# Kernel tuning notes

Hardware: AMD Instinct MI355X
Metric: run time of the kernel (lower is better)

The kernel has to match this reference:

```python
import jax, jax.numpy as jnp
import numpy as np

EPS = 1e-7
NUM_ROUTINGS = 3


def squash(s):
    # s: [..., V]; maps norm into [0, 1)
    norm = jnp.linalg.norm(s, axis=-1, keepdims=True)
    coef = norm ** 2 / (norm ** 2 + 1.0)
    return coef * s / (norm + EPS)


def setup_inputs() -> dict:
    key = jax.random.key(0)
    k1, k2 = jax.random.split(key)
    B, N, Q = 32, 32768, 8          # batch, num_primary, dim_primary
    D, V = 10, 16                   # num_digit, dim_digit
    primary_caps = jax.random.normal(k1, (B, N, Q), dtype=jnp.float32)
    # glorot-ish scale for W [num_digit, num_primary, dim_digit, dim_primary]
    W = jax.random.normal(k2, (D, N, V, Q), dtype=jnp.float32) * (1.0 / np.sqrt(Q))
    return {"primary_caps": primary_caps, "W": W}


def reference(primary_caps, W):
    # u_hat[b,d,n,v] = sum_q W[d,n,v,q] * u[b,n,q]  -> [B, D, N, V]
    u_hat = jnp.einsum("dnvq,bnq->bdnv", W, primary_caps)
    B, D, N, V = u_hat.shape
    b = jnp.zeros((B, D, N), dtype=u_hat.dtype)
    v = None
    for r in range(NUM_ROUTINGS):
        c = jax.nn.softmax(b, axis=1)                      # softmax over digit axis
        s = jnp.einsum("bdn,bdnv->bdv", c, u_hat)          # [B, D, V]
        v = squash(s)                                      # [B, D, V]
        if r < NUM_ROUTINGS - 1:
            b = b + jnp.einsum("bdnv,bdv->bdn", u_hat, v)  # agreement update
    return v  # [B, num_digit, dim_digit]
```

## Files before the change

kernel.cpp:

```cpp
#include <hip/hip_runtime.h>

namespace {
constexpr int kB = 32;
constexpr int kN = 32768;
constexpr int kQ = 8;
constexpr int kD = 10;
constexpr int kV = 16;
constexpr int kRows = kB * kD;
constexpr int kThreads = 512;
constexpr int kGrid = 1024;
constexpr int kNPB = kN / kGrid;
}

template <int CTRL>
__device__ __forceinline__ float dpp_mv(float x) {
  return __int_as_float(__builtin_amdgcn_update_dpp(
      0, __float_as_int(x), CTRL, 0xF, 0xF, true));
}

template <int PHASE>
__launch_bounds__(kThreads, 2)
__global__ void routing_pass(const float* __restrict__ u,
                             const float* __restrict__ W,
                             const float* __restrict__ vprev,
                             float* __restrict__ s_out) {
  const int t = threadIdx.x;
  const int ln = t & 63;
  const int dslot = ln >> 2;
  const int vq = ln & 3;
  const bool act = (dslot < kD);
  const int dd = act ? dslot : dslot - kD;
  const int b0 = (t >> 6) * 4;

  float vp[4][4];
  if constexpr (PHASE != 0) {
    #pragma unroll
    for (int bb = 0; bb < 4; ++bb)
      #pragma unroll
      for (int j = 0; j < 4; ++j)
        vp[bb][j] = vprev[((b0 + bb) * kD + dd) * kV + j * 4 + vq];
  }

  float acc[4][4];
  #pragma unroll
  for (int bb = 0; bb < 4; ++bb)
    #pragma unroll
    for (int j = 0; j < 4; ++j) acc[bb][j] = 0.0f;

  const int n_base = blockIdx.x * kNPB;
  const char* wbase = (const char*)W + ((size_t)dd * kN + n_base) * 512 + vq * 32;
  const int ub = b0 + ((ln & 31) >> 3);
  const float* ubase = u + ((size_t)ub * kN + n_base + (ln >> 5)) * kQ + (ln & 7);

  for (int g = 0; g < kNPB / 4; ++g) {
    const float r0 = ubase[(g * 4 + 0) * kQ];
    const float r1 = ubase[(g * 4 + 2) * kQ];
    #pragma unroll
    for (int nl = 0; nl < 4; ++nl) {
      const float upair = (nl < 2) ? r0 : r1;
      const int hb = (nl & 1) * 32;
      const char* wn = wbase + (size_t)(g * 4 + nl) * 512;

      float uh[4][4];
      #pragma unroll
      for (int bb = 0; bb < 4; ++bb)
        #pragma unroll
        for (int j = 0; j < 4; ++j) uh[bb][j] = 0.0f;

      #pragma unroll
      for (int qh = 0; qh < 2; ++qh) {
        float us[4][4];
        #pragma unroll
        for (int bb = 0; bb < 4; ++bb)
          #pragma unroll
          for (int ql = 0; ql < 4; ++ql)
            us[bb][ql] = __int_as_float(__builtin_amdgcn_readlane(
                __float_as_int(upair), hb + bb * 8 + qh * 4 + ql));
        #pragma unroll
        for (int j = 0; j < 4; ++j) {
          const float4 w4 = *(const float4*)(wn + j * 128 + qh * 16);
          #pragma unroll
          for (int bb = 0; bb < 4; ++bb) {
            uh[bb][j] = fmaf(w4.x, us[bb][0], uh[bb][j]);
            uh[bb][j] = fmaf(w4.y, us[bb][1], uh[bb][j]);
            uh[bb][j] = fmaf(w4.z, us[bb][2], uh[bb][j]);
            uh[bb][j] = fmaf(w4.w, us[bb][3], uh[bb][j]);
          }
        }
      }
      if constexpr (PHASE != 0) {
        float lg[4];
        #pragma unroll
        for (int bb = 0; bb < 4; ++bb) {
          float t0 = uh[bb][0] * vp[bb][0];
          t0 = fmaf(uh[bb][1], vp[bb][1], t0);
          t0 = fmaf(uh[bb][2], vp[bb][2], t0);
          t0 = fmaf(uh[bb][3], vp[bb][3], t0);
          t0 += dpp_mv<0xB1>(t0);
          t0 += dpp_mv<0x4E>(t0);
          lg[bb] = t0;
        }
        const float ta = (vq & 2) ? lg[2] : lg[0];
        const float tb = (vq & 2) ? lg[3] : lg[1];
        const float lsel = (vq & 1) ? tb : ta;
        const float esel = act ? __expf(lsel) : 0.0f;
        float den = esel;
        den += dpp_mv<0x124>(den);
        den += dpp_mv<0x128>(den);
        den += __shfl_xor(den, 16);
        den += __shfl_xor(den, 32);
        const float csel = esel * __builtin_amdgcn_rcpf(den);
        const float cb[4] = {dpp_mv<0x00>(csel), dpp_mv<0x55>(csel),
                             dpp_mv<0xAA>(csel), dpp_mv<0xFF>(csel)};
        #pragma unroll
        for (int bb = 0; bb < 4; ++bb)
          #pragma unroll
          for (int j = 0; j < 4; ++j)
            acc[bb][j] = fmaf(cb[bb], uh[bb][j], acc[bb][j]);
      } else {
        #pragma unroll
        for (int bb = 0; bb < 4; ++bb)
          #pragma unroll
          for (int j = 0; j < 4; ++j) acc[bb][j] += uh[bb][j];
      }
    }
  }

  if (act) {
    const float scale = (PHASE == 0) ? 0.1f : 1.0f;
    #pragma unroll
    for (int bb = 0; bb < 4; ++bb) {
      float* srow = s_out + ((b0 + bb) * kD + dslot) * kV + vq;
      #pragma unroll
      for (int j = 0; j < 4; ++j)
        atomicAdd(&srow[j * 4], acc[bb][j] * scale);
    }
  }
}

template <int MODE>
__global__ void squash_kernel(float* __restrict__ s,
                              float* __restrict__ vprev,
                              float* __restrict__ out) {
  const int t = threadIdx.x;
  if (t >= kRows) return;
  float* sr = s + t * kV;
  float sv[kV];
  float n2 = 0.0f;
  #pragma unroll
  for (int v = 0; v < kV; ++v) {
    sv[v] = sr[v];
    n2 = fmaf(sv[v], sv[v], n2);
  }
  if (MODE != 2) {
    #pragma unroll
    for (int v = 0; v < kV; ++v) sr[v] = 0.0f;
  }
  const float norm = sqrtf(n2);
  const float coef = n2 / ((n2 + 1.0f) * (norm + 1e-7f));
  float* dst = (MODE == 2) ? (out + t * kV) : (vprev + t * kV);
  #pragma unroll
  for (int v = 0; v < kV; ++v) {
    float val = coef * sv[v];
    if (MODE == 1) val += dst[v];
    dst[v] = val;
  }
}

extern "C" void kernel_launch(void* const* d_in, const int* in_sizes, int n_in,
                              void* d_out, int out_size, void* d_ws, size_t ws_size,
                              hipStream_t stream) {
  const float* u = reinterpret_cast<const float*>(d_in[0]);
  const float* W = reinterpret_cast<const float*>(d_in[1]);
  float* out = reinterpret_cast<float*>(d_out);

  float* s = reinterpret_cast<float*>(d_ws);
  float* vprev = s + kRows * kV;
  const size_t sbytes = (size_t)kRows * kV * sizeof(float);

  (void)hipMemsetAsync(s, 0, sbytes, stream);
  routing_pass<0><<<kGrid, kThreads, 0, stream>>>(u, W, nullptr, s);
  squash_kernel<0><<<1, kThreads, 0, stream>>>(s, vprev, out);

  routing_pass<1><<<kGrid, kThreads, 0, stream>>>(u, W, vprev, s);
  squash_kernel<1><<<1, kThreads, 0, stream>>>(s, vprev, out);

  routing_pass<1><<<kGrid, kThreads, 0, stream>>>(u, W, vprev, s);
  squash_kernel<2><<<1, kThreads, 0, stream>>>(s, vprev, out);
}
```

Before: 618.7 us.

## Split batch across two blocks per N-partition to halve per-thread register tiles

Each block now handles 16 of the 32 batch rows (2 per wave instead of 4), doubling the grid and halving accumulator and u_hat register arrays, with launch bounds raised to 4 blocks per CU. This aims to improve occupancy and latency hiding. The cost is that every W tile is read twice (once per batch half), doubling W traffic, plus more atomics to the output.

```diff
diff --git a/kernel.cpp b/kernel.cpp
--- a/kernel.cpp
+++ b/kernel.cpp
@@ -8,8 +8,10 @@
 constexpr int kV = 16;
 constexpr int kRows = kB * kD;
 constexpr int kThreads = 512;
-constexpr int kGrid = 1024;
-constexpr int kNPB = kN / kGrid;
+constexpr int kParts = 1024;
+constexpr int kGrid = kParts * 2;
+constexpr int kNPB = kN / kParts;
+constexpr int kG = kNPB / 4;
 }
 
 template <int CTRL>
@@ -19,7 +21,7 @@
 }
 
 template <int PHASE>
-__launch_bounds__(kThreads, 2)
+__launch_bounds__(kThreads, 4)
 __global__ void routing_pass(const float* __restrict__ u,
                              const float* __restrict__ W,
                              const float* __restrict__ vprev,
@@ -30,57 +32,55 @@
   const int vq = ln & 3;
   const bool act = (dslot < kD);
   const int dd = act ? dslot : dslot - kD;
-  const int b0 = (t >> 6) * 4;
+  const int bg = blockIdx.x & 1;
+  const int part = blockIdx.x >> 1;
+  const int b0 = bg * 16 + (t >> 6) * 2;
+  const int n_base = part * kNPB;
 
-  float vp[4][4];
+  float vp[2][4];
   if constexpr (PHASE != 0) {
     #pragma unroll
-    for (int bb = 0; bb < 4; ++bb)
+    for (int bb = 0; bb < 2; ++bb)
       #pragma unroll
       for (int j = 0; j < 4; ++j)
         vp[bb][j] = vprev[((b0 + bb) * kD + dd) * kV + j * 4 + vq];
   }
 
-  float acc[4][4];
+  float acc[2][4];
   #pragma unroll
-  for (int bb = 0; bb < 4; ++bb)
+  for (int bb = 0; bb < 2; ++bb)
     #pragma unroll
     for (int j = 0; j < 4; ++j) acc[bb][j] = 0.0f;
 
-  const int n_base = blockIdx.x * kNPB;
   const char* wbase = (const char*)W + ((size_t)dd * kN + n_base) * 512 + vq * 32;
-  const int ub = b0 + ((ln & 31) >> 3);
-  const float* ubase = u + ((size_t)ub * kN + n_base + (ln >> 5)) * kQ + (ln & 7);
+  const float* ubase = u + ((size_t)(b0 + (ln >> 5)) * kN + n_base + ((ln >> 3) & 3)) * kQ
+                       + (ln & 7);
 
-  for (int g = 0; g < kNPB / 4; ++g) {
-    const float r0 = ubase[(g * 4 + 0) * kQ];
-    const float r1 = ubase[(g * 4 + 2) * kQ];
+  for (int g = 0; g < kG; ++g) {
+    const float ureg = ubase[g * 4 * kQ];
     #pragma unroll
     for (int nl = 0; nl < 4; ++nl) {
-      const float upair = (nl < 2) ? r0 : r1;
-      const int hb = (nl & 1) * 32;
       const char* wn = wbase + (size_t)(g * 4 + nl) * 512;
-
-      float uh[4][4];
+      float uh[2][4];
       #pragma unroll
-      for (int bb = 0; bb < 4; ++bb)
+      for (int bb = 0; bb < 2; ++bb)
         #pragma unroll
         for (int j = 0; j < 4; ++j) uh[bb][j] = 0.0f;
 
       #pragma unroll
       for (int qh = 0; qh < 2; ++qh) {
-        float us[4][4];
+        float us[2][4];
         #pragma unroll
-        for (int bb = 0; bb < 4; ++bb)
+        for (int bb = 0; bb < 2; ++bb)
           #pragma unroll
           for (int ql = 0; ql < 4; ++ql)
             us[bb][ql] = __int_as_float(__builtin_amdgcn_readlane(
-                __float_as_int(upair), hb + bb * 8 + qh * 4 + ql));
+                __float_as_int(ureg), bb * 32 + nl * 8 + qh * 4 + ql));
         #pragma unroll
         for (int j = 0; j < 4; ++j) {
           const float4 w4 = *(const float4*)(wn + j * 128 + qh * 16);
           #pragma unroll
-          for (int bb = 0; bb < 4; ++bb) {
+          for (int bb = 0; bb < 2; ++bb) {
             uh[bb][j] = fmaf(w4.x, us[bb][0], uh[bb][j]);
             uh[bb][j] = fmaf(w4.y, us[bb][1], uh[bb][j]);
             uh[bb][j] = fmaf(w4.z, us[bb][2], uh[bb][j]);
@@ -88,10 +88,11 @@
           }
         }
       }
+
       if constexpr (PHASE != 0) {
-        float lg[4];
+        float lg[2];
         #pragma unroll
-        for (int bb = 0; bb < 4; ++bb) {
+        for (int bb = 0; bb < 2; ++bb) {
           float t0 = uh[bb][0] * vp[bb][0];
           t0 = fmaf(uh[bb][1], vp[bb][1], t0);
           t0 = fmaf(uh[bb][2], vp[bb][2], t0);
@@ -100,9 +101,7 @@
           t0 += dpp_mv<0x4E>(t0);
           lg[bb] = t0;
         }
-        const float ta = (vq & 2) ? lg[2] : lg[0];
-        const float tb = (vq & 2) ? lg[3] : lg[1];
-        const float lsel = (vq & 1) ? tb : ta;
+        const float lsel = (vq & 2) ? lg[1] : lg[0];
         const float esel = act ? __expf(lsel) : 0.0f;
         float den = esel;
         den += dpp_mv<0x124>(den);
@@ -110,16 +109,16 @@
         den += __shfl_xor(den, 16);
         den += __shfl_xor(den, 32);
         const float csel = esel * __builtin_amdgcn_rcpf(den);
-        const float cb[4] = {dpp_mv<0x00>(csel), dpp_mv<0x55>(csel),
-                             dpp_mv<0xAA>(csel), dpp_mv<0xFF>(csel)};
+        const float cb0 = dpp_mv<0x00>(csel);
+        const float cb1 = dpp_mv<0xAA>(csel);
         #pragma unroll
-        for (int bb = 0; bb < 4; ++bb)
-          #pragma unroll
-          for (int j = 0; j < 4; ++j)
-            acc[bb][j] = fmaf(cb[bb], uh[bb][j], acc[bb][j]);
+        for (int j = 0; j < 4; ++j) {
+          acc[0][j] = fmaf(cb0, uh[0][j], acc[0][j]);
+          acc[1][j] = fmaf(cb1, uh[1][j], acc[1][j]);
+        }
       } else {
         #pragma unroll
-        for (int bb = 0; bb < 4; ++bb)
+        for (int bb = 0; bb < 2; ++bb)
           #pragma unroll
           for (int j = 0; j < 4; ++j) acc[bb][j] += uh[bb][j];
       }
@@ -129,7 +128,7 @@
   if (act) {
     const float scale = (PHASE == 0) ? 0.1f : 1.0f;
     #pragma unroll
-    for (int bb = 0; bb < 4; ++bb) {
+    for (int bb = 0; bb < 2; ++bb) {
       float* srow = s_out + ((b0 + bb) * kD + dslot) * kV + vq;
       #pragma unroll
       for (int j = 0; j < 4; ++j)
```

After: 971.9 us. 57.1% more time.
